# Kernel tuning notes

Hardware: AMD Instinct MI355X
Metric: run time of the kernel (lower is better)

## Reference

```python
import jax, jax.numpy as jnp
import numpy as np

MARGIN = 0.1


def setup_inputs() -> dict:
    key = jax.random.key(0)
    k1, k2 = jax.random.split(key)
    N, M, C = 16384, 16384, 512
    return {
        "features_view1": jax.random.normal(k1, (N, C), dtype=jnp.float32),
        "features_view2": jax.random.normal(k2, (M, C), dtype=jnp.float32),
    }


def reference(features_view1, features_view2):
    # torch.cdist(p=2) via the matmul identity ||a-b||^2 = |a|^2 + |b|^2 - 2 a.b
    sq1 = jnp.sum(features_view1 * features_view1, axis=1, keepdims=True)  # [N,1]
    sq2 = jnp.sum(features_view2 * features_view2, axis=1)                 # [M]
    inner = features_view1 @ features_view2.T                              # [N,M]
    dist2 = jnp.maximum(sq1 + sq2[None, :] - 2.0 * inner, 0.0)
    nn_dist = jnp.sqrt(jnp.min(dist2, axis=1))                             # [N]
    return jnp.mean(jax.nn.relu(nn_dist - MARGIN))
```

## Files before the change

### kernel.cpp

```cpp
#include <hip/hip_runtime.h>
#include <stdint.h>

#define N_ROWS 16384
#define M_ROWS 16384
#define KDIM   512
#define BM 128
#define BNT 64
#define BKP 128
#define NCHUNK 8
#define CHUNK_ROWS (M_ROWS / NCHUNK)
#define BT_PER_CHUNK (CHUNK_ROWS / BNT)

typedef int intx4 __attribute__((ext_vector_type(4)));
typedef int intx8 __attribute__((ext_vector_type(8)));
typedef float floatx4 __attribute__((ext_vector_type(4)));

#define UNIT_SCALE 0x7F7F7F7F

__device__ __forceinline__ void async_ld16(const uint8_t* g, uint8_t* l) {
  __builtin_amdgcn_global_load_lds(
      (const __attribute__((address_space(1))) void*)g,
      (__attribute__((address_space(3))) void*)l, 16, 0, 0);
}

__global__ void conv_kernel(const float* __restrict__ A, const float* __restrict__ B,
                            uint8_t* __restrict__ Ah8, uint8_t* __restrict__ Bh8,
                            float* __restrict__ sq1, float* __restrict__ sq2) {
  const int lane = threadIdx.x & 63;
  const int wv = threadIdx.x >> 6;
  int row = blockIdx.x * 4 + wv;
  const float* src;
  uint8_t* dst;
  float* sq;
  if (row < N_ROWS) {
    src = A + (size_t)row * KDIM;
    dst = Ah8 + (size_t)row * KDIM;
    sq = sq1 + row;
  } else {
    int r = row - N_ROWS;
    src = B + (size_t)r * KDIM;
    dst = Bh8 + (size_t)r * KDIM;
    sq = sq2 + r;
  }
  const float4* s4 = (const float4*)src;
  float4 v0 = s4[lane * 2];
  float4 v1 = s4[lane * 2 + 1];
  uint32_t w0 = 0, w1 = 0;
  w0 = __builtin_amdgcn_cvt_pk_fp8_f32(v0.x, v0.y, w0, 0);
  w0 = __builtin_amdgcn_cvt_pk_fp8_f32(v0.z, v0.w, w0, 1);
  w1 = __builtin_amdgcn_cvt_pk_fp8_f32(v1.x, v1.y, w1, 0);
  w1 = __builtin_amdgcn_cvt_pk_fp8_f32(v1.z, v1.w, w1, 1);
  uint2 pk = {w0, w1};
  ((uint2*)dst)[lane] = pk;
  float s = v0.x * v0.x + v0.y * v0.y + v0.z * v0.z + v0.w * v0.w
          + v1.x * v1.x + v1.y * v1.y + v1.z * v1.z + v1.w * v1.w;
  #pragma unroll
  for (int off = 32; off; off >>= 1) s += __shfl_down(s, off, 64);
  if (lane == 0) *sq = s;
}

__global__ void __launch_bounds__(128, 2)
gemm_min_kernel(const uint8_t* __restrict__ Ah8, const uint8_t* __restrict__ Bh8,
                const float* __restrict__ sq2, float* __restrict__ ws_min) {
  __shared__ __align__(16) uint8_t lsB[4][BNT * BKP];
  __shared__ __align__(16) float sq2_lds[CHUNK_ROWS];

  const int tid = threadIdx.x;
  const int lane = tid & 63;
  const int wv = tid >> 6;
  const int fr = lane & 15;
  const int kg = lane >> 4;
  const int frs = fr & 7;

  const int bid = blockIdx.x;
  const int chunk = bid & 7;
  const int rowBase = (bid >> 3) * BM;
  const int colBase0 = chunk * CHUNK_ROWS;

  const int cis = lane >> 3;
  const int kofs_st = (((lane & 7) ^ cis) << 4);

  intx8 areg[4][4];
  {
    const uint8_t* abase = Ah8 + (size_t)(rowBase + wv * 64 + fr) * KDIM + kg * 32;
    #pragma unroll
    for (int i = 0; i < 4; i++)
      #pragma unroll
      for (int p = 0; p < 4; p++) {
        const uint8_t* ap = abase + (size_t)i * 16 * KDIM + p * BKP;
        intx4 lo = *(const intx4*)ap;
        intx4 hi = *(const intx4*)(ap + 16);
        areg[i][p] = __builtin_shufflevector(lo, hi, 0, 1, 2, 3, 4, 5, 6, 7);
      }
  }

  float runmin[4][4];
  #pragma unroll
  for (int i = 0; i < 4; i++)
    #pragma unroll
    for (int r4 = 0; r4 < 4; r4++) runmin[i][r4] = 3.0e38f;

  #define STAGE_B(buf, cb, kbase_)                                            \
    {                                                                         \
      _Pragma("unroll")                                                       \
      for (int c = 0; c < 4; ++c) {                                           \
        const int slot = wv * 4 + c;                                          \
        async_ld16(Bh8 + (size_t)((cb) + slot * 8 + cis) * KDIM +             \
                       (kbase_) + kofs_st,                                    \
                   (buf) + (slot << 10));                                     \
      }                                                                       \
    }

  {
    const uint8_t* s2src = (const uint8_t*)(sq2 + colBase0);
    #pragma unroll
    for (int c = 0; c < 4; ++c) {
      const int off = ((wv * 4 + c) << 10);
      async_ld16(s2src + off + lane * 16, ((uint8_t*)sq2_lds) + off);
    }
  }
  STAGE_B(lsB[0], colBase0, 0)
  STAGE_B(lsB[1], colBase0, BKP)
  STAGE_B(lsB[2], colBase0, 2 * BKP)

  for (int bt = 0; bt < BT_PER_CHUNK; ++bt) {
    const int colBase = colBase0 + bt * BNT;
    floatx4 acc[4][4];
    #pragma unroll
    for (int i = 0; i < 4; i++)
      #pragma unroll
      for (int j = 0; j < 4; j++) acc[i][j] = (floatx4){0.f, 0.f, 0.f, 0.f};

    #pragma unroll
    for (int p = 0; p < 4; ++p) {
      if (p >= 2 && bt == BT_PER_CHUNK - 1) {
        if (p == 2) {
          asm volatile("s_waitcnt vmcnt(4)" ::: "memory");
        } else {
          asm volatile("s_waitcnt vmcnt(0)" ::: "memory");
        }
      } else {
        asm volatile("s_waitcnt vmcnt(8)" ::: "memory");
      }
      __builtin_amdgcn_s_barrier();
      asm volatile("" ::: "memory");
      __builtin_amdgcn_sched_barrier(0);

      if (p == 0) {
        STAGE_B(lsB[3], colBase, 3 * BKP)
      } else if (bt + 1 < BT_PER_CHUNK) {
        STAGE_B(lsB[(p + 3) & 3], colBase + BNT, (p - 1) * BKP)
      }

      const uint8_t* cur = lsB[p];
      __builtin_amdgcn_s_setprio(1);
      #pragma unroll
      for (int j = 0; j < 4; j++) {
        const uint8_t* bp = cur + (j * 16 + fr) * BKP;
        intx4 lo = *(const intx4*)(bp + ((((kg << 1)) ^ frs) << 4));
        intx4 hi = *(const intx4*)(bp + ((((kg << 1) | 1) ^ frs) << 4));
        intx8 bv = __builtin_shufflevector(lo, hi, 0, 1, 2, 3, 4, 5, 6, 7);
        #pragma unroll
        for (int i = 0; i < 4; i++)
          acc[i][j] = __builtin_amdgcn_mfma_scale_f32_16x16x128_f8f6f4(
              areg[i][p], bv, acc[i][j], 0, 0,
              0, UNIT_SCALE, 0, UNIT_SCALE);
      }
      __builtin_amdgcn_s_setprio(0);
    }

    #pragma unroll
    for (int j = 0; j < 4; j++) {
      const float s2 = sq2_lds[bt * BNT + j * 16 + fr];
      #pragma unroll
      for (int i = 0; i < 4; i++)
        #pragma unroll
        for (int r4 = 0; r4 < 4; r4++) {
          const float cand = fmaf(-2.f, acc[i][j][r4], s2);
          runmin[i][r4] = fminf(runmin[i][r4], cand);
        }
    }
  }

  #pragma unroll
  for (int i = 0; i < 4; i++)
    #pragma unroll
    for (int r4 = 0; r4 < 4; r4++) {
      float v = runmin[i][r4];
      v = fminf(v, __shfl_xor(v, 1, 64));
      v = fminf(v, __shfl_xor(v, 2, 64));
      v = fminf(v, __shfl_xor(v, 4, 64));
      v = fminf(v, __shfl_xor(v, 8, 64));
      runmin[i][r4] = v;
    }

  if (fr == 0) {
    #pragma unroll
    for (int i = 0; i < 4; i++)
      #pragma unroll
      for (int r4 = 0; r4 < 4; r4++) {
        const int lrow = wv * 64 + i * 16 + kg * 4 + r4;
        ws_min[(size_t)chunk * N_ROWS + rowBase + lrow] = runmin[i][r4];
      }
  }
}

__global__ void partial_kernel(const float* __restrict__ ws_min,
                               const float* __restrict__ sq1,
                               float* __restrict__ part) {
  const int r = blockIdx.x * 256 + threadIdx.x;
  float m = ws_min[r];
  #pragma unroll
  for (int c = 1; c < NCHUNK; c++) m = fminf(m, ws_min[(size_t)c * N_ROWS + r]);
  float d2 = sq1[r] + m;
  d2 = d2 > 0.f ? d2 : 0.f;
  float v = sqrtf(d2) - 0.1f;
  float s = v > 0.f ? v : 0.f;
  #pragma unroll
  for (int off = 32; off; off >>= 1) s += __shfl_down(s, off, 64);
  __shared__ float ps[4];
  if ((threadIdx.x & 63) == 0) ps[threadIdx.x >> 6] = s;
  __syncthreads();
  if (threadIdx.x == 0) part[blockIdx.x] = ps[0] + ps[1] + ps[2] + ps[3];
}

__global__ void final_kernel(const float* __restrict__ part, float* __restrict__ out) {
  float s = part[threadIdx.x];
  #pragma unroll
  for (int off = 32; off; off >>= 1) s += __shfl_down(s, off, 64);
  if (threadIdx.x == 0) out[0] = s / (float)N_ROWS;
}

extern "C" void kernel_launch(void* const* d_in, const int* in_sizes, int n_in,
                              void* d_out, int out_size, void* d_ws, size_t ws_size,
                              hipStream_t stream) {
  const float* A = (const float*)d_in[0];
  const float* B = (const float*)d_in[1];
  char* ws = (char*)d_ws;
  const size_t fp8Bytes = (size_t)N_ROWS * KDIM;
  uint8_t* Ah8 = (uint8_t*)ws;
  uint8_t* Bh8 = (uint8_t*)(ws + fp8Bytes);
  float* sq1 = (float*)(ws + 2 * fp8Bytes);
  float* sq2 = sq1 + N_ROWS;
  float* ws_min = sq2 + M_ROWS;
  float* part = ws_min + (size_t)NCHUNK * N_ROWS;

  conv_kernel<<<dim3((N_ROWS + M_ROWS) / 4), dim3(256), 0, stream>>>(A, B, Ah8, Bh8, sq1, sq2);
  gemm_min_kernel<<<dim3((N_ROWS / BM) * NCHUNK), dim3(128), 0, stream>>>(Ah8, Bh8, sq2, ws_min);
  partial_kernel<<<dim3(64), dim3(256), 0, stream>>>(ws_min, sq1, part);
  final_kernel<<<dim3(1), dim3(64), 0, stream>>>(part, (float*)d_out);
}
```

Baseline: 207.9 us.

## Double the GEMM row tile to four waves and double-buffer whole B tiles

The row tile per block grows from 128 to 256 rows using four waves, so each B tile staged in LDS is shared by twice as many rows. The four-slot pipeline that staged one k-slice per phase is replaced by two buffers, each holding a full 64x512 B tile, with one wait and barrier per column tile instead of four. This cuts the total B traffic, but each block now waits for a whole tile before computing, which gives coarser overlap, and the block uses more LDS and may fit fewer blocks per CU.

Result: faster. 191.9 us (-7.7%).

```diff
diff --git a/kernel.cpp b/kernel.cpp
--- a/kernel.cpp
+++ b/kernel.cpp
@@ -4,7 +4,7 @@
 #define N_ROWS 16384
 #define M_ROWS 16384
 #define KDIM   512
-#define BM 128
+#define BM 256
 #define BNT 64
 #define BKP 128
 #define NCHUNK 8
@@ -59,10 +59,10 @@
   if (lane == 0) *sq = s;
 }
 
-__global__ void __launch_bounds__(128, 2)
+__global__ void __launch_bounds__(256, 2)
 gemm_min_kernel(const uint8_t* __restrict__ Ah8, const uint8_t* __restrict__ Bh8,
                 const float* __restrict__ sq2, float* __restrict__ ws_min) {
-  __shared__ __align__(16) uint8_t lsB[4][BNT * BKP];
+  __shared__ __align__(16) uint8_t lsB[2][4 * BNT * BKP];
   __shared__ __align__(16) float sq2_lds[CHUNK_ROWS];
 
   const int tid = threadIdx.x;
@@ -100,63 +100,52 @@
     #pragma unroll
     for (int r4 = 0; r4 < 4; r4++) runmin[i][r4] = 3.0e38f;
 
-  #define STAGE_B(buf, cb, kbase_)                                            \
+  #define STAGE_TILE(buf, cb)                                                 \
     {                                                                         \
       _Pragma("unroll")                                                       \
-      for (int c = 0; c < 4; ++c) {                                           \
-        const int slot = wv * 4 + c;                                          \
-        async_ld16(Bh8 + (size_t)((cb) + slot * 8 + cis) * KDIM +             \
-                       (kbase_) + kofs_st,                                    \
-                   (buf) + (slot << 10));                                     \
+      for (int p_ = 0; p_ < 4; ++p_) {                                        \
+        _Pragma("unroll")                                                     \
+        for (int c_ = 0; c_ < 2; ++c_) {                                      \
+          const int slot = wv * 2 + c_;                                       \
+          async_ld16(Bh8 + (size_t)((cb) + slot * 8 + cis) * KDIM +           \
+                         p_ * BKP + kofs_st,                                  \
+                     (buf) + p_ * (BNT * BKP) + (slot << 10));                \
+        }                                                                     \
       }                                                                       \
     }
 
   {
     const uint8_t* s2src = (const uint8_t*)(sq2 + colBase0);
     #pragma unroll
-    for (int c = 0; c < 4; ++c) {
-      const int off = ((wv * 4 + c) << 10);
+    for (int c = 0; c < 2; ++c) {
+      const int off = ((wv * 2 + c) << 10);
       async_ld16(s2src + off + lane * 16, ((uint8_t*)sq2_lds) + off);
     }
   }
-  STAGE_B(lsB[0], colBase0, 0)
-  STAGE_B(lsB[1], colBase0, BKP)
-  STAGE_B(lsB[2], colBase0, 2 * BKP)
+  STAGE_TILE(lsB[0], colBase0)
 
   for (int bt = 0; bt < BT_PER_CHUNK; ++bt) {
-    const int colBase = colBase0 + bt * BNT;
+    asm volatile("s_waitcnt vmcnt(0)" ::: "memory");
+    __builtin_amdgcn_s_barrier();
+    __builtin_amdgcn_sched_barrier(0);
+
+    if (bt + 1 < BT_PER_CHUNK) {
+      STAGE_TILE(lsB[(bt + 1) & 1], colBase0 + (bt + 1) * BNT)
+    }
+
+    const uint8_t* cur = lsB[bt & 1];
     floatx4 acc[4][4];
     #pragma unroll
     for (int i = 0; i < 4; i++)
       #pragma unroll
       for (int j = 0; j < 4; j++) acc[i][j] = (floatx4){0.f, 0.f, 0.f, 0.f};
 
+    __builtin_amdgcn_s_setprio(1);
     #pragma unroll
     for (int p = 0; p < 4; ++p) {
-      if (p >= 2 && bt == BT_PER_CHUNK - 1) {
-        if (p == 2) {
-          asm volatile("s_waitcnt vmcnt(4)" ::: "memory");
-        } else {
-          asm volatile("s_waitcnt vmcnt(0)" ::: "memory");
-        }
-      } else {
-        asm volatile("s_waitcnt vmcnt(8)" ::: "memory");
-      }
-      __builtin_amdgcn_s_barrier();
-      asm volatile("" ::: "memory");
-      __builtin_amdgcn_sched_barrier(0);
-
-      if (p == 0) {
-        STAGE_B(lsB[3], colBase, 3 * BKP)
-      } else if (bt + 1 < BT_PER_CHUNK) {
-        STAGE_B(lsB[(p + 3) & 3], colBase + BNT, (p - 1) * BKP)
-      }
-
-      const uint8_t* cur = lsB[p];
-      __builtin_amdgcn_s_setprio(1);
-      #pragma unroll
-      for (int j = 0; j < 4; j++) {
-        const uint8_t* bp = cur + (j * 16 + fr) * BKP;
+      #pragma unroll
+      for (int j = 0; j < 4; ++j) {
+        const uint8_t* bp = cur + p * (BNT * BKP) + (j * 16 + fr) * BKP;
         intx4 lo = *(const intx4*)(bp + ((((kg << 1)) ^ frs) << 4));
         intx4 hi = *(const intx4*)(bp + ((((kg << 1) | 1) ^ frs) << 4));
         intx8 bv = __builtin_shufflevector(lo, hi, 0, 1, 2, 3, 4, 5, 6, 7);
@@ -166,8 +155,8 @@
               areg[i][p], bv, acc[i][j], 0, 0,
               0, UNIT_SCALE, 0, UNIT_SCALE);
       }
-      __builtin_amdgcn_s_setprio(0);
-    }
+    }
+    __builtin_amdgcn_s_setprio(0);
 
     #pragma unroll
     for (int j = 0; j < 4; j++) {
@@ -246,7 +235,7 @@
   float* part = ws_min + (size_t)NCHUNK * N_ROWS;
 
   conv_kernel<<<dim3((N_ROWS + M_ROWS) / 4), dim3(256), 0, stream>>>(A, B, Ah8, Bh8, sq1, sq2);
-  gemm_min_kernel<<<dim3((N_ROWS / BM) * NCHUNK), dim3(128), 0, stream>>>(Ah8, Bh8, sq2, ws_min);
+  gemm_min_kernel<<<dim3((N_ROWS / BM) * NCHUNK), dim3(256), 0, stream>>>(Ah8, Bh8, sq2, ws_min);
   partial_kernel<<<dim3(64), dim3(256), 0, stream>>>(ws_min, sq1, part);
   final_kernel<<<dim3(1), dim3(64), 0, stream>>>(part, (float*)d_out);
 }
```
